# Optimization experiments

Hardware: AMD Instinct MI355X
Metric: run time of the kernel (lower is better)

Reference implementation:

```python
import jax, jax.numpy as jnp
import numpy as np

B, C, H, W = 4, 128, 128, 128
CO = 128           # output channels of deformable conv
KH = KW = 3
K = KH * KW        # 9 kernel taps


def setup_inputs() -> dict:
    key = jax.random.key(0)
    k1, k2, k3, k4 = jax.random.split(key, 4)
    x = jax.random.normal(k1, (B, C, H, W), jnp.float32)
    # conv_offset: Conv2D(3*K channels, 3x3, stride 1, same, bias), channels_first
    offset_w = jax.random.normal(k2, (3 * K, C, KH, KW), jnp.float32) * 0.01
    offset_b = jnp.zeros((3 * K,), jnp.float32)
    # deformable conv weights: [CO, C, KH, KW] + bias
    deform_w = jax.random.normal(k3, (CO, C, KH, KW), jnp.float32) * (1.0 / np.sqrt(C * K))
    deform_b = jax.random.normal(k4, (CO,), jnp.float32) * 0.01
    return {"x": x, "offset_w": offset_w, "offset_b": offset_b,
            "deform_w": deform_w, "deform_b": deform_b}


def _bilinear_gather(x, y, xc):
    """Bilinear sample x [B,C,H,W] at float coords y, xc [B,K,H,W].
    Out-of-bounds samples contribute zero. Returns [B,C,K,H,W]."""
    Bn, Cn, Hn, Wn = x.shape
    y0 = jnp.floor(y)
    x0 = jnp.floor(xc)
    wy = y - y0   # frac weights
    wx = xc - x0
    xf = x.reshape(Bn, Cn, Hn * Wn)

    def corner(yc, xcc, wgt):
        valid = (yc >= 0) & (yc < Hn) & (xcc >= 0) & (xcc < Wn)
        yi = jnp.clip(yc, 0, Hn - 1).astype(jnp.int32)
        xi = jnp.clip(xcc, 0, Wn - 1).astype(jnp.int32)
        idx = (yi * Wn + xi).reshape(Bn, 1, -1)            # [B,1,K*H*W]
        g = jnp.take_along_axis(xf, idx, axis=2)           # [B,C,K*H*W]
        g = g.reshape(Bn, Cn, *yc.shape[1:])               # [B,C,K,H,W]
        return g * (wgt * valid)[:, None]

    return (corner(y0,     x0,     (1 - wy) * (1 - wx))
          + corner(y0,     x0 + 1, (1 - wy) * wx)
          + corner(y0 + 1, x0,     wy * (1 - wx))
          + corner(y0 + 1, x0 + 1, wy * wx))


def reference(x, offset_w, offset_b, deform_w, deform_b):
    # offset/mask predicting conv (stride 1, SAME, channels_first)
    wi = jax.lax.conv_general_dilated(
        x, offset_w, window_strides=(1, 1), padding='SAME',
        dimension_numbers=('NCHW', 'OIHW', 'NCHW')) + offset_b[None, :, None, None]
    o1, o2, m = jnp.split(wi, 3, axis=1)      # each [B,K,H,W]
    dy, dx = o1, o2                            # offset = concat(o1, o2)
    mask = jax.nn.sigmoid(m)

    # kernel tap displacements relative to center (SAME padding, 3x3)
    ky = jnp.repeat(jnp.arange(KH), KW) - (KH // 2)   # [K]
    kx = jnp.tile(jnp.arange(KW), KH) - (KW // 2)     # [K]
    y = dy + jnp.arange(H, dtype=jnp.float32)[None, None, :, None] + ky[None, :, None, None]
    xs = dx + jnp.arange(W, dtype=jnp.float32)[None, None, None, :] + kx[None, :, None, None]

    samp = _bilinear_gather(x, y, xs)          # [B,C,K,H,W]
    # modulated accumulation: sum over ci and kernel taps
    out = jnp.einsum('bckhw,ock->bohw', samp * mask[:, None], deform_w.reshape(CO, C, K))
    return out + deform_b[None, :, None, None]
```

## Files before the change

### kernel.cpp

```cpp
#include <hip/hip_runtime.h>
#include <math.h>

#define Bn 4
#define Cn 128
#define Hn 128
#define Wn 128
#define COn 128
#define HWn (Hn*Wn)
#define NPIX (Bn*HWn)

typedef __attribute__((ext_vector_type(8))) short bf16x8;
typedef __attribute__((ext_vector_type(4))) float f32x4;

__device__ inline short f2bf(float f) {
    union { float f; unsigned u; } cv; cv.f = f;
    unsigned u = cv.u;
    u += 0x7fffu + ((u >> 16) & 1u);
    return (short)(u >> 16);
}
__device__ inline float bflo(unsigned w) {
    union { unsigned u; float f; } cv; cv.u = w << 16; return cv.f;
}
__device__ inline float bfhi(unsigned w) {
    union { unsigned u; float f; } cv; cv.u = w & 0xffff0000u; return cv.f;
}
__device__ inline void async_copy16(const void* g, void* l) {
    __builtin_amdgcn_global_load_lds(
        (const __attribute__((address_space(1))) unsigned int*)g,
        (__attribute__((address_space(3))) unsigned int*)l, 16, 0, 0);
}

__global__ __launch_bounds__(256) void k_transpose(
    const float* __restrict__ x, unsigned short* __restrict__ xt)
{
    __shared__ unsigned short t[Wn][Cn + 2];
    const int tid = threadIdx.x;
    const int bh  = blockIdx.x;
    const int b   = bh >> 7, h = bh & 127;
    const float* xp = x + (((size_t)b*Cn) << 14) + h*Wn;
    for (int i = tid; i < Cn*Wn; i += 256) {
        int c = i >> 7, w = i & 127;
        t[w][c] = (unsigned short)f2bf(xp[(size_t)c*HWn + w]);
    }
    __syncthreads();
    unsigned* xto = (unsigned*)(xt + ((size_t)bh << 7) * Cn);
    for (int j = tid; j < Wn*(Cn/2); j += 256) {
        int w = j >> 6, cp = j & 63;
        xto[(size_t)w*64 + cp] = *(const unsigned*)&t[w][2*cp];
    }
}

__global__ __launch_bounds__(64) void k_pack_w(
    const float* __restrict__ dw, short* __restrict__ pw)
{
    const int blk = blockIdx.x;
    const int ks  = blk >> 3;
    const int ot  = blk & 7;
    const int cchunk = ks / 9;
    const int tap    = ks - cchunk*9;
    const int l   = threadIdx.x;
    const int oc  = ot*16 + (l & 15);
    const int kk0 = (l >> 4)*8;
    bf16x8 fr;
    #pragma unroll
    for (int j = 0; j < 8; ++j) {
        int c = cchunk*32 + kk0 + j;
        fr[j] = f2bf(dw[oc*1152 + c*9 + tap]);
    }
    *(bf16x8*)(pw + ((size_t)blk*64 + l)*8) = fr;
}

__global__ __launch_bounds__(64) void k_pack_ow(
    const float* __restrict__ ow, short* __restrict__ pwo)
{
    const int blk = blockIdx.x;
    const int ks  = blk >> 1;
    const int ot  = blk & 1;
    const int cchunk = ks / 9;
    const int tap    = ks - cchunk*9;
    const int l   = threadIdx.x;
    const int oc  = ot*16 + (l & 15);
    const int kk0 = (l >> 4)*8;
    bf16x8 fr;
    #pragma unroll
    for (int j = 0; j < 8; ++j) {
        int c = cchunk*32 + kk0 + j;
        fr[j] = (oc < 27) ? f2bf(ow[oc*1152 + c*9 + tap]) : (short)0;
    }
    *(bf16x8*)(pwo + ((size_t)blk*64 + l)*8) = fr;
}

__global__ __launch_bounds__(256) void k_offset_mfma(
    const unsigned short* __restrict__ xt, const short* __restrict__ pwo,
    const float* __restrict__ ob, float* __restrict__ offs)
{
    const int tid = threadIdx.x;
    const int wid = tid >> 6;
    const int l   = tid & 63;
    const int lm  = l & 15;
    const int lg  = l >> 4;
    const int bid = blockIdx.x;
    const int wg  = (bid & 7)*128 + (bid >> 3);
    const int p   = wg*64 + wid*16 + lm;
    const int b   = p >> 14;
    const int hw  = p & (HWn - 1);
    const int h   = hw >> 7;
    const int w   = hw & (Wn - 1);

    f32x4 acc[2];
    acc[0] = (f32x4){0.f,0.f,0.f,0.f};
    acc[1] = (f32x4){0.f,0.f,0.f,0.f};
    const int4* apg = (const int4*)pwo;

    #pragma unroll 1
    for (int ks = 0; ks < 36; ++ks) {
        const int cchunk = ks / 9;
        const int tap    = ks - cchunk*9;
        const int y  = h + tap/3 - 1;
        const int xx = w + (tap - (tap/3)*3) - 1;
        const bool ok = (y >= 0) & (y < Hn) & (xx >= 0) & (xx < Wn);
        const int yc  = min(max(y, 0), Hn-1);
        const int xc  = min(max(xx, 0), Wn-1);
        int4 v = *(const int4*)(xt + (((size_t)(b*Hn + yc)*Wn + xc) << 7)
                                   + cchunk*32 + lg*8);
        if (!ok) v = make_int4(0,0,0,0);
        const int4* ap = apg + (size_t)(ks*2)*64 + l;
        acc[0] = __builtin_amdgcn_mfma_f32_16x16x32_bf16(
            __builtin_bit_cast(bf16x8, ap[0]), __builtin_bit_cast(bf16x8, v), acc[0], 0, 0, 0);
        acc[1] = __builtin_amdgcn_mfma_f32_16x16x32_bf16(
            __builtin_bit_cast(bf16x8, ap[64]), __builtin_bit_cast(bf16x8, v), acc[1], 0, 0, 0);
    }

    #pragma unroll
    for (int ot = 0; ot < 2; ++ot)
        #pragma unroll
        for (int r = 0; r < 4; ++r) {
            int oc = ot*16 + lg*4 + r;
            if (oc < 27) offs[(size_t)p*27 + oc] = acc[ot][r] + ob[oc];
        }
}

__global__ __launch_bounds__(256) void k_deform_mfma(
    const unsigned short* __restrict__ xt, const char* __restrict__ pw,
    const float* __restrict__ db, const float* __restrict__ offs,
    float* __restrict__ out)
{
    __shared__ __align__(16) char a_lds[2][8192];
    const int tid = threadIdx.x;
    const int wid = tid >> 6;
    const int l   = tid & 63;
    const int lm  = l & 15;
    const int lg  = l >> 4;
    const int bid = blockIdx.x;
    const int wg  = (bid & 7)*128 + (bid >> 3);
    const int p   = wg*64 + wid*16 + lm;
    const int b   = p >> 14;
    const int hw  = p & (HWn - 1);
    const int h   = hw >> 7;
    const int w   = hw & (Wn - 1);

    f32x4 acc[8];
    #pragma unroll
    for (int ot = 0; ot < 8; ++ot) acc[ot] = (f32x4){0.f,0.f,0.f,0.f};

    const float* op = offs + (size_t)p * 27;
    const int rowbase = b*Hn;

    #define STAGE(ks_, buf_) {                                                  \
        const char* g0 = pw + (size_t)(ks_)*8192 + wid*1024 + l*16;             \
        async_copy16(g0,        (void*)&a_lds[buf_][wid*1024]);                 \
        async_copy16(g0 + 4096, (void*)&a_lds[buf_][4096 + wid*1024]);          \
    }

    STAGE(0, 0);
    int cur = 0;

    #pragma unroll 1
    for (int ks = 0; ks < 36; ++ks) {
        const int cchunk = ks / 9;
        const int tap    = ks - cchunk*9;
        __syncthreads();
        if (ks + 1 < 36) STAGE(ks + 1, cur ^ 1);

        float dy = op[tap], dx = op[9 + tap], mr = op[18 + tap];
        float m  = 1.0f / (1.0f + __expf(-mr));
        float yf = (float)(h + tap/3 - 1) + dy;
        float xf = (float)(w + (tap - (tap/3)*3) - 1) + dx;
        float y0f = floorf(yf), x0f = floorf(xf);
        int   y0  = (int)y0f,  x0  = (int)x0f;
        float wy = yf - y0f, wx = xf - x0f;
        int yi0 = min(max(y0,     0), Hn-1), yi1 = min(max(y0 + 1, 0), Hn-1);
        int xi0 = min(max(x0,     0), Wn-1), xi1 = min(max(x0 + 1, 0), Wn-1);
        float vy0 = ((y0 >= 0)     & (y0 < Hn))     ? 1.0f : 0.0f;
        float vy1 = ((y0 + 1 >= 0) & (y0 + 1 < Hn)) ? 1.0f : 0.0f;
        float vx0 = ((x0 >= 0)     & (x0 < Wn))     ? 1.0f : 0.0f;
        float vx1 = ((x0 + 1 >= 0) & (x0 + 1 < Wn)) ? 1.0f : 0.0f;
        const float w0_ = m * (1.0f-wy) * (1.0f-wx) * vy0 * vx0;
        const float w1_ = m * (1.0f-wy) * wx        * vy0 * vx1;
        const float w2_ = m * wy        * (1.0f-wx) * vy1 * vx0;
        const float w3_ = m * wy        * wx        * vy1 * vx1;

        const int cb = cchunk*32 + lg*8;
        const uint4 q0 = *(const uint4*)(xt + (((size_t)((rowbase + yi0)*Wn + xi0)) << 7) + cb);
        const uint4 q1 = *(const uint4*)(xt + (((size_t)((rowbase + yi0)*Wn + xi1)) << 7) + cb);
        const uint4 q2 = *(const uint4*)(xt + (((size_t)((rowbase + yi1)*Wn + xi0)) << 7) + cb);
        const uint4 q3 = *(const uint4*)(xt + (((size_t)((rowbase + yi1)*Wn + xi1)) << 7) + cb);

        unsigned bw[4];
        const unsigned* u0 = (const unsigned*)&q0;
        const unsigned* u1 = (const unsigned*)&q1;
        const unsigned* u2 = (const unsigned*)&q2;
        const unsigned* u3 = (const unsigned*)&q3;
        #pragma unroll
        for (int q = 0; q < 4; ++q) {
            float lo = w0_*bflo(u0[q]) + w1_*bflo(u1[q]) + w2_*bflo(u2[q]) + w3_*bflo(u3[q]);
            float hi = w0_*bfhi(u0[q]) + w1_*bfhi(u1[q]) + w2_*bfhi(u2[q]) + w3_*bfhi(u3[q]);
            bw[q] = ((unsigned)(unsigned short)f2bf(hi) << 16) | (unsigned short)f2bf(lo);
        }
        int4 bi = make_int4(bw[0], bw[1], bw[2], bw[3]);
        bf16x8 bfrag = __builtin_bit_cast(bf16x8, bi);

        #pragma unroll
        for (int ot = 0; ot < 8; ++ot) {
            int4 av = *(const int4*)&a_lds[cur][(ot*64 + l)*16];
            acc[ot] = __builtin_amdgcn_mfma_f32_16x16x32_bf16(
                __builtin_bit_cast(bf16x8, av), bfrag, acc[ot], 0, 0, 0);
        }
        cur ^= 1;
    }

    #pragma unroll
    for (int ot = 0; ot < 8; ++ot) {
        #pragma unroll
        for (int r = 0; r < 4; ++r) {
            int oc = ot*16 + lg*4 + r;
            out[((size_t)(b*COn + oc) << 14) + hw] = acc[ot][r] + db[oc];
        }
    }
    #undef STAGE
}

extern "C" void kernel_launch(void* const* d_in, const int* in_sizes, int n_in,
                              void* d_out, int out_size, void* d_ws, size_t ws_size,
                              hipStream_t stream) {
    const float* x  = (const float*)d_in[0];
    const float* ow = (const float*)d_in[1];
    const float* ob = (const float*)d_in[2];
    const float* dw = (const float*)d_in[3];
    const float* db = (const float*)d_in[4];
    float* out  = (float*)d_out;

    float*          offs = (float*)d_ws;
    short*          pw   = (short*)((char*)d_ws + 7077888);
    short*          pwo  = (short*)((char*)d_ws + 7372800);
    unsigned short* xtp  = (unsigned short*)((char*)d_ws + 7446528);

    hipLaunchKernelGGL(k_transpose,   dim3(Bn*Hn),    dim3(256), 0, stream, x, xtp);
    hipLaunchKernelGGL(k_pack_w,      dim3(288),      dim3(64),  0, stream, dw, pw);
    hipLaunchKernelGGL(k_pack_ow,     dim3(72),       dim3(64),  0, stream, ow, pwo);
    hipLaunchKernelGGL(k_offset_mfma, dim3(NPIX/64),  dim3(256), 0, stream, xtp, pwo, ob, offs);
    hipLaunchKernelGGL(k_deform_mfma, dim3(NPIX/64),  dim3(256), 0, stream,
                       xtp, (const char*)pw, db, offs, out);
}
```

Measured before the change: 137.4 us.

## Reorder K loop tap-major so bilinear coords are computed once per tap

The reduction loop now runs over taps outermost with the four 32-channel chunks innermost. Packed weights are reordered to match the new tap-major index. Offset, mask and bilinear weights are computed once per tap instead of once per chunk, and the four corner gathers for one pixel hit consecutive channel chunks, which should improve locality. The software bf16 conversion is also replaced with the HIP intrinsic, which may lower to a hardware convert; rounding should stay round-to-nearest-even.

```diff
diff --git a/kernel.cpp b/kernel.cpp
--- a/kernel.cpp
+++ b/kernel.cpp
@@ -1,4 +1,5 @@
 #include <hip/hip_runtime.h>
+#include <hip/hip_bf16.h>
 #include <math.h>
 
 #define Bn 4
@@ -12,11 +13,15 @@
 typedef __attribute__((ext_vector_type(8))) short bf16x8;
 typedef __attribute__((ext_vector_type(4))) float f32x4;
 
-__device__ inline short f2bf(float f) {
-    union { float f; unsigned u; } cv; cv.f = f;
-    unsigned u = cv.u;
-    u += 0x7fffu + ((u >> 16) & 1u);
-    return (short)(u >> 16);
+__device__ inline unsigned short f2bf_hw(float f) {
+    __hip_bfloat16 h = __float2bfloat16(f);
+    return *reinterpret_cast<unsigned short*>(&h);
+}
+__device__ inline unsigned pack_bf2(float lo, float hi) {
+    __hip_bfloat162 h2;
+    h2.x = __float2bfloat16(lo);
+    h2.y = __float2bfloat16(hi);
+    return *reinterpret_cast<unsigned*>(&h2);
 }
 __device__ inline float bflo(unsigned w) {
     union { unsigned u; float f; } cv; cv.u = w << 16; return cv.f;
@@ -40,7 +45,7 @@
     const float* xp = x + (((size_t)b*Cn) << 14) + h*Wn;
     for (int i = tid; i < Cn*Wn; i += 256) {
         int c = i >> 7, w = i & 127;
-        t[w][c] = (unsigned short)f2bf(xp[(size_t)c*HWn + w]);
+        t[w][c] = f2bf_hw(xp[(size_t)c*HWn + w]);
     }
     __syncthreads();
     unsigned* xto = (unsigned*)(xt + ((size_t)bh << 7) * Cn);
@@ -56,16 +61,16 @@
     const int blk = blockIdx.x;
     const int ks  = blk >> 3;
     const int ot  = blk & 7;
-    const int cchunk = ks / 9;
-    const int tap    = ks - cchunk*9;
+    const int tap = ks >> 2;
+    const int cq  = ks & 3;
     const int l   = threadIdx.x;
     const int oc  = ot*16 + (l & 15);
     const int kk0 = (l >> 4)*8;
     bf16x8 fr;
     #pragma unroll
     for (int j = 0; j < 8; ++j) {
-        int c = cchunk*32 + kk0 + j;
-        fr[j] = f2bf(dw[oc*1152 + c*9 + tap]);
+        int c = cq*32 + kk0 + j;
+        fr[j] = (short)f2bf_hw(dw[oc*1152 + c*9 + tap]);
     }
     *(bf16x8*)(pw + ((size_t)blk*64 + l)*8) = fr;
 }
@@ -76,16 +81,16 @@
     const int blk = blockIdx.x;
     const int ks  = blk >> 1;
     const int ot  = blk & 1;
-    const int cchunk = ks / 9;
-    const int tap    = ks - cchunk*9;
+    const int tap = ks >> 2;
+    const int cq  = ks & 3;
     const int l   = threadIdx.x;
     const int oc  = ot*16 + (l & 15);
     const int kk0 = (l >> 4)*8;
     bf16x8 fr;
     #pragma unroll
     for (int j = 0; j < 8; ++j) {
-        int c = cchunk*32 + kk0 + j;
-        fr[j] = (oc < 27) ? f2bf(ow[oc*1152 + c*9 + tap]) : (short)0;
+        int c = cq*32 + kk0 + j;
+        fr[j] = (oc < 27) ? (short)f2bf_hw(ow[oc*1152 + c*9 + tap]) : (short)0;
     }
     *(bf16x8*)(pwo + ((size_t)blk*64 + l)*8) = fr;
 }
@@ -113,22 +118,25 @@
     const int4* apg = (const int4*)pwo;
 
     #pragma unroll 1
-    for (int ks = 0; ks < 36; ++ks) {
-        const int cchunk = ks / 9;
-        const int tap    = ks - cchunk*9;
+    for (int tap = 0; tap < 9; ++tap) {
         const int y  = h + tap/3 - 1;
         const int xx = w + (tap - (tap/3)*3) - 1;
         const bool ok = (y >= 0) & (y < Hn) & (xx >= 0) & (xx < Wn);
         const int yc  = min(max(y, 0), Hn-1);
         const int xc  = min(max(xx, 0), Wn-1);
-        int4 v = *(const int4*)(xt + (((size_t)(b*Hn + yc)*Wn + xc) << 7)
-                                   + cchunk*32 + lg*8);
-        if (!ok) v = make_int4(0,0,0,0);
-        const int4* ap = apg + (size_t)(ks*2)*64 + l;
-        acc[0] = __builtin_amdgcn_mfma_f32_16x16x32_bf16(
-            __builtin_bit_cast(bf16x8, ap[0]), __builtin_bit_cast(bf16x8, v), acc[0], 0, 0, 0);
-        acc[1] = __builtin_amdgcn_mfma_f32_16x16x32_bf16(
-            __builtin_bit_cast(bf16x8, ap[64]), __builtin_bit_cast(bf16x8, v), acc[1], 0, 0, 0);
+        const unsigned short* bp =
+            xt + (((size_t)((b*Hn + yc)*Wn + xc)) << 7) + lg*8;
+        #pragma unroll
+        for (int cq = 0; cq < 4; ++cq) {
+            int4 v = *(const int4*)(bp + cq*32);
+            if (!ok) v = make_int4(0,0,0,0);
+            const int ks = tap*4 + cq;
+            const int4* ap = apg + (size_t)(ks*2)*64 + l;
+            acc[0] = __builtin_amdgcn_mfma_f32_16x16x32_bf16(
+                __builtin_bit_cast(bf16x8, ap[0]),  __builtin_bit_cast(bf16x8, v), acc[0], 0, 0, 0);
+            acc[1] = __builtin_amdgcn_mfma_f32_16x16x32_bf16(
+                __builtin_bit_cast(bf16x8, ap[64]), __builtin_bit_cast(bf16x8, v), acc[1], 0, 0, 0);
+        }
     }
 
     #pragma unroll
@@ -176,12 +184,7 @@
     int cur = 0;
 
     #pragma unroll 1
-    for (int ks = 0; ks < 36; ++ks) {
-        const int cchunk = ks / 9;
-        const int tap    = ks - cchunk*9;
-        __syncthreads();
-        if (ks + 1 < 36) STAGE(ks + 1, cur ^ 1);
-
+    for (int tap = 0; tap < 9; ++tap) {
         float dy = op[tap], dx = op[9 + tap], mr = op[18 + tap];
         float m  = 1.0f / (1.0f + __expf(-mr));
         float yf = (float)(h + tap/3 - 1) + dy;
@@ -200,33 +203,44 @@
         const float w2_ = m * wy        * (1.0f-wx) * vy1 * vx0;
         const float w3_ = m * wy        * wx        * vy1 * vx1;
 
-        const int cb = cchunk*32 + lg*8;
-        const uint4 q0 = *(const uint4*)(xt + (((size_t)((rowbase + yi0)*Wn + xi0)) << 7) + cb);
-        const uint4 q1 = *(const uint4*)(xt + (((size_t)((rowbase + yi0)*Wn + xi1)) << 7) + cb);
-        const uint4 q2 = *(const uint4*)(xt + (((size_t)((rowbase + yi1)*Wn + xi0)) << 7) + cb);
-        const uint4 q3 = *(const uint4*)(xt + (((size_t)((rowbase + yi1)*Wn + xi1)) << 7) + cb);
-
-        unsigned bw[4];
-        const unsigned* u0 = (const unsigned*)&q0;
-        const unsigned* u1 = (const unsigned*)&q1;
-        const unsigned* u2 = (const unsigned*)&q2;
-        const unsigned* u3 = (const unsigned*)&q3;
-        #pragma unroll
-        for (int q = 0; q < 4; ++q) {
-            float lo = w0_*bflo(u0[q]) + w1_*bflo(u1[q]) + w2_*bflo(u2[q]) + w3_*bflo(u3[q]);
-            float hi = w0_*bfhi(u0[q]) + w1_*bfhi(u1[q]) + w2_*bfhi(u2[q]) + w3_*bfhi(u3[q]);
-            bw[q] = ((unsigned)(unsigned short)f2bf(hi) << 16) | (unsigned short)f2bf(lo);
-        }
-        int4 bi = make_int4(bw[0], bw[1], bw[2], bw[3]);
-        bf16x8 bfrag = __builtin_bit_cast(bf16x8, bi);
-
-        #pragma unroll
-        for (int ot = 0; ot < 8; ++ot) {
-            int4 av = *(const int4*)&a_lds[cur][(ot*64 + l)*16];
-            acc[ot] = __builtin_amdgcn_mfma_f32_16x16x32_bf16(
-                __builtin_bit_cast(bf16x8, av), bfrag, acc[ot], 0, 0, 0);
-        }
-        cur ^= 1;
+        const unsigned short* c00 = xt + (((size_t)((rowbase + yi0)*Wn + xi0)) << 7) + lg*8;
+        const unsigned short* c01 = xt + (((size_t)((rowbase + yi0)*Wn + xi1)) << 7) + lg*8;
+        const unsigned short* c10 = xt + (((size_t)((rowbase + yi1)*Wn + xi0)) << 7) + lg*8;
+        const unsigned short* c11 = xt + (((size_t)((rowbase + yi1)*Wn + xi1)) << 7) + lg*8;
+
+        #pragma unroll
+        for (int cq = 0; cq < 4; ++cq) {
+            const int ks = tap*4 + cq;
+            __syncthreads();
+            if (ks + 1 < 36) STAGE(ks + 1, cur ^ 1);
+
+            const uint4 q0 = *(const uint4*)(c00 + cq*32);
+            const uint4 q1 = *(const uint4*)(c01 + cq*32);
+            const uint4 q2 = *(const uint4*)(c10 + cq*32);
+            const uint4 q3 = *(const uint4*)(c11 + cq*32);
+
+            unsigned bw[4];
+            const unsigned* u0 = (const unsigned*)&q0;
+            const unsigned* u1 = (const unsigned*)&q1;
+            const unsigned* u2 = (const unsigned*)&q2;
+            const unsigned* u3 = (const unsigned*)&q3;
+            #pragma unroll
+            for (int q = 0; q < 4; ++q) {
+                float lo = w0_*bflo(u0[q]) + w1_*bflo(u1[q]) + w2_*bflo(u2[q]) + w3_*bflo(u3[q]);
+                float hi = w0_*bfhi(u0[q]) + w1_*bfhi(u1[q]) + w2_*bfhi(u2[q]) + w3_*bfhi(u3[q]);
+                bw[q] = pack_bf2(lo, hi);
+            }
+            int4 bi = make_int4(bw[0], bw[1], bw[2], bw[3]);
+            bf16x8 bfrag = __builtin_bit_cast(bf16x8, bi);
+
+            #pragma unroll
+            for (int ot = 0; ot < 8; ++ot) {
+                int4 av = *(const int4*)&a_lds[cur][(ot*64 + l)*16];
+                acc[ot] = __builtin_amdgcn_mfma_f32_16x16x32_bf16(
+                    __builtin_bit_cast(bf16x8, av), bfrag, acc[ot], 0, 0, 0);
+            }
+            cur ^= 1;
+        }
     }
 
     #pragma unroll
```

After: 151.1 us. 10.0% more time.

## Split deform conv K-loop across two wave groups with LDS reduction

Applied to the files above, without the earlier changes.

The deformable conv kernel now runs 512 threads per block. Two groups of four waves each handle half of the 36 k-steps, each with its own double-buffered weight staging in LDS, and the partial accumulators are summed through LDS before the output store. This doubles the waves working on each 64-pixel tile, shortening the serial gather-plus-MFMA chain per wave and adding latency hiding, at the cost of double the LDS, a reduction step, and idle waves during the store. The manual float-to-bf16 rounding is also replaced with the HIP intrinsic conversion, which may lower to hardware pack instructions.

```diff
diff --git a/kernel.cpp b/kernel.cpp
--- a/kernel.cpp
+++ b/kernel.cpp
@@ -1,4 +1,5 @@
 #include <hip/hip_runtime.h>
+#include <hip/hip_bf16.h>
 #include <math.h>
 
 #define Bn 4
@@ -12,11 +13,15 @@
 typedef __attribute__((ext_vector_type(8))) short bf16x8;
 typedef __attribute__((ext_vector_type(4))) float f32x4;
 
-__device__ inline short f2bf(float f) {
-    union { float f; unsigned u; } cv; cv.f = f;
-    unsigned u = cv.u;
-    u += 0x7fffu + ((u >> 16) & 1u);
-    return (short)(u >> 16);
+__device__ inline unsigned short f2bf_hw(float f) {
+    __hip_bfloat16 h = __float2bfloat16(f);
+    return *reinterpret_cast<unsigned short*>(&h);
+}
+__device__ inline unsigned pack_bf2(float lo, float hi) {
+    __hip_bfloat162 h2;
+    h2.x = __float2bfloat16(lo);
+    h2.y = __float2bfloat16(hi);
+    return *reinterpret_cast<unsigned*>(&h2);
 }
 __device__ inline float bflo(unsigned w) {
     union { unsigned u; float f; } cv; cv.u = w << 16; return cv.f;
@@ -40,7 +45,7 @@
     const float* xp = x + (((size_t)b*Cn) << 14) + h*Wn;
     for (int i = tid; i < Cn*Wn; i += 256) {
         int c = i >> 7, w = i & 127;
-        t[w][c] = (unsigned short)f2bf(xp[(size_t)c*HWn + w]);
+        t[w][c] = f2bf_hw(xp[(size_t)c*HWn + w]);
     }
     __syncthreads();
     unsigned* xto = (unsigned*)(xt + ((size_t)bh << 7) * Cn);
@@ -65,7 +70,7 @@
     #pragma unroll
     for (int j = 0; j < 8; ++j) {
         int c = cchunk*32 + kk0 + j;
-        fr[j] = f2bf(dw[oc*1152 + c*9 + tap]);
+        fr[j] = (short)f2bf_hw(dw[oc*1152 + c*9 + tap]);
     }
     *(bf16x8*)(pw + ((size_t)blk*64 + l)*8) = fr;
 }
@@ -85,7 +90,7 @@
     #pragma unroll
     for (int j = 0; j < 8; ++j) {
         int c = cchunk*32 + kk0 + j;
-        fr[j] = (oc < 27) ? f2bf(ow[oc*1152 + c*9 + tap]) : (short)0;
+        fr[j] = (oc < 27) ? (short)f2bf_hw(ow[oc*1152 + c*9 + tap]) : (short)0;
     }
     *(bf16x8*)(pwo + ((size_t)blk*64 + l)*8) = fr;
 }
@@ -126,7 +131,7 @@
         if (!ok) v = make_int4(0,0,0,0);
         const int4* ap = apg + (size_t)(ks*2)*64 + l;
         acc[0] = __builtin_amdgcn_mfma_f32_16x16x32_bf16(
-            __builtin_bit_cast(bf16x8, ap[0]), __builtin_bit_cast(bf16x8, v), acc[0], 0, 0, 0);
+            __builtin_bit_cast(bf16x8, ap[0]),  __builtin_bit_cast(bf16x8, v), acc[0], 0, 0, 0);
         acc[1] = __builtin_amdgcn_mfma_f32_16x16x32_bf16(
             __builtin_bit_cast(bf16x8, ap[64]), __builtin_bit_cast(bf16x8, v), acc[1], 0, 0, 0);
     }
@@ -140,24 +145,26 @@
         }
 }
 
-__global__ __launch_bounds__(256) void k_deform_mfma(
+__global__ __launch_bounds__(512, 8) void k_deform_mfma(
     const unsigned short* __restrict__ xt, const char* __restrict__ pw,
     const float* __restrict__ db, const float* __restrict__ offs,
     float* __restrict__ out)
 {
-    __shared__ __align__(16) char a_lds[2][8192];
-    const int tid = threadIdx.x;
-    const int wid = tid >> 6;
-    const int l   = tid & 63;
-    const int lm  = l & 15;
-    const int lg  = l >> 4;
-    const int bid = blockIdx.x;
-    const int wg  = (bid & 7)*128 + (bid >> 3);
-    const int p   = wg*64 + wid*16 + lm;
-    const int b   = p >> 14;
-    const int hw  = p & (HWn - 1);
-    const int h   = hw >> 7;
-    const int w   = hw & (Wn - 1);
+    __shared__ __align__(16) char a_lds[2][2][8192];
+    const int tid  = threadIdx.x;
+    const int wid  = tid >> 6;
+    const int gid  = wid >> 2;
+    const int wsub = wid & 3;
+    const int l    = tid & 63;
+    const int lm   = l & 15;
+    const int lg   = l >> 4;
+    const int bid  = blockIdx.x;
+    const int wg   = (bid & 7)*128 + (bid >> 3);
+    const int p    = wg*64 + wsub*16 + lm;
+    const int b    = p >> 14;
+    const int hw   = p & (HWn - 1);
+    const int h    = hw >> 7;
+    const int w    = hw & (Wn - 1);
 
     f32x4 acc[8];
     #pragma unroll
@@ -165,22 +172,24 @@
 
     const float* op = offs + (size_t)p * 27;
     const int rowbase = b*Hn;
+    const int ks0 = gid*18;
 
     #define STAGE(ks_, buf_) {                                                  \
-        const char* g0 = pw + (size_t)(ks_)*8192 + wid*1024 + l*16;             \
-        async_copy16(g0,        (void*)&a_lds[buf_][wid*1024]);                 \
-        async_copy16(g0 + 4096, (void*)&a_lds[buf_][4096 + wid*1024]);          \
-    }
-
-    STAGE(0, 0);
+        const char* g0 = pw + (size_t)(ks_)*8192 + wsub*1024 + l*16;            \
+        async_copy16(g0,        (void*)&a_lds[gid][buf_][wsub*1024]);           \
+        async_copy16(g0 + 4096, (void*)&a_lds[gid][buf_][4096 + wsub*1024]);    \
+    }
+
+    STAGE(ks0, 0);
     int cur = 0;
 
     #pragma unroll 1
-    for (int ks = 0; ks < 36; ++ks) {
+    for (int s = 0; s < 18; ++s) {
+        const int ks     = ks0 + s;
         const int cchunk = ks / 9;
         const int tap    = ks - cchunk*9;
         __syncthreads();
-        if (ks + 1 < 36) STAGE(ks + 1, cur ^ 1);
+        if (s + 1 < 18) STAGE(ks + 1, cur ^ 1);
 
         float dy = op[tap], dx = op[9 + tap], mr = op[18 + tap];
         float m  = 1.0f / (1.0f + __expf(-mr));
@@ -215,29 +224,40 @@
         for (int q = 0; q < 4; ++q) {
             float lo = w0_*bflo(u0[q]) + w1_*bflo(u1[q]) + w2_*bflo(u2[q]) + w3_*bflo(u3[q]);
             float hi = w0_*bfhi(u0[q]) + w1_*bfhi(u1[q]) + w2_*bfhi(u2[q]) + w3_*bfhi(u3[q]);
-            bw[q] = ((unsigned)(unsigned short)f2bf(hi) << 16) | (unsigned short)f2bf(lo);
+            bw[q] = pack_bf2(lo, hi);
         }
         int4 bi = make_int4(bw[0], bw[1], bw[2], bw[3]);
         bf16x8 bfrag = __builtin_bit_cast(bf16x8, bi);
 
         #pragma unroll
         for (int ot = 0; ot < 8; ++ot) {
-            int4 av = *(const int4*)&a_lds[cur][(ot*64 + l)*16];
+            int4 av = *(const int4*)&a_lds[gid][cur][(ot*64 + l)*16];
             acc[ot] = __builtin_amdgcn_mfma_f32_16x16x32_bf16(
                 __builtin_bit_cast(bf16x8, av), bfrag, acc[ot], 0, 0, 0);
         }
         cur ^= 1;
     }
-
-    #pragma unroll
-    for (int ot = 0; ot < 8; ++ot) {
-        #pragma unroll
-        for (int r = 0; r < 4; ++r) {
-            int oc = ot*16 + lg*4 + r;
-            out[((size_t)(b*COn + oc) << 14) + hw] = acc[ot][r] + db[oc];
-        }
-    }
     #undef STAGE
+
+    __syncthreads();
+    float4* red = (float4*)a_lds;
+    if (gid == 1) {
+        #pragma unroll
+        for (int ot = 0; ot < 8; ++ot)
+            red[(wsub*8 + ot)*64 + l] = (float4){acc[ot][0], acc[ot][1], acc[ot][2], acc[ot][3]};
+    }
+    __syncthreads();
+    if (gid == 0) {
+        #pragma unroll
+        for (int ot = 0; ot < 8; ++ot) {
+            float4 o2 = red[(wsub*8 + ot)*64 + l];
+            #pragma unroll
+            for (int r = 0; r < 4; ++r) {
+                int oc = ot*16 + lg*4 + r;
+                out[((size_t)(b*COn + oc) << 14) + hw] = acc[ot][r] + (&o2.x)[r] + db[oc];
+            }
+        }
+    }
 }
 
 extern "C" void kernel_launch(void* const* d_in, const int* in_sizes, int n_in,
@@ -259,6 +279,6 @@
     hipLaunchKernelGGL(k_pack_w,      dim3(288),      dim3(64),  0, stream, dw, pw);
     hipLaunchKernelGGL(k_pack_ow,     dim3(72),       dim3(64),  0, stream, ow, pwo);
     hipLaunchKernelGGL(k_offset_mfma, dim3(NPIX/64),  dim3(256), 0, stream, xtp, pwo, ob, offs);
-    hipLaunchKernelGGL(k_deform_mfma, dim3(NPIX/64),  dim3(256), 0, stream,
+    hipLaunchKernelGGL(k_deform_mfma, dim3(NPIX/64),  dim3(512), 0, stream,
                        xtp, (const char*)pw, db, offs, out);
 }
```

Result: slower. 184.6 us (+34.3%).

## Precompute bilinear sampling metadata in offset kernel, use hardware bf16 conversion

Applied to the files above, without the earlier changes.

The offset conv kernel now stages its outputs in LDS and computes per-pixel, per-tap sampling metadata: a base byte offset, neighbour step flags, and four bf16-packed bilinear weights with the mask folded in. This replaces the float offset buffer. The deform kernel previously redid this sigmoid, floor and clamp work for each of the 4 channel chunks; it now loads one 16-byte record per tap instead. Float-to-bf16 conversion also switches to the HIP intrinsic, which may map to a packed hardware convert. The cost is that bilinear weights are quantized to bf16, a small precision change, and the metadata buffer is larger than the old offsets buffer.

```diff
diff --git a/kernel.cpp b/kernel.cpp
--- a/kernel.cpp
+++ b/kernel.cpp
@@ -1,4 +1,5 @@
 #include <hip/hip_runtime.h>
+#include <hip/hip_bf16.h>
 #include <math.h>
 
 #define Bn 4
@@ -12,11 +13,15 @@
 typedef __attribute__((ext_vector_type(8))) short bf16x8;
 typedef __attribute__((ext_vector_type(4))) float f32x4;
 
-__device__ inline short f2bf(float f) {
-    union { float f; unsigned u; } cv; cv.f = f;
-    unsigned u = cv.u;
-    u += 0x7fffu + ((u >> 16) & 1u);
-    return (short)(u >> 16);
+__device__ inline unsigned short f2bf_hw(float f) {
+    __hip_bfloat16 h = __float2bfloat16(f);
+    return *reinterpret_cast<unsigned short*>(&h);
+}
+__device__ inline unsigned pack_bf2(float lo, float hi) {
+    __hip_bfloat162 h2;
+    h2.x = __float2bfloat16(lo);
+    h2.y = __float2bfloat16(hi);
+    return *reinterpret_cast<unsigned*>(&h2);
 }
 __device__ inline float bflo(unsigned w) {
     union { unsigned u; float f; } cv; cv.u = w << 16; return cv.f;
@@ -40,7 +45,7 @@
     const float* xp = x + (((size_t)b*Cn) << 14) + h*Wn;
     for (int i = tid; i < Cn*Wn; i += 256) {
         int c = i >> 7, w = i & 127;
-        t[w][c] = (unsigned short)f2bf(xp[(size_t)c*HWn + w]);
+        t[w][c] = f2bf_hw(xp[(size_t)c*HWn + w]);
     }
     __syncthreads();
     unsigned* xto = (unsigned*)(xt + ((size_t)bh << 7) * Cn);
@@ -65,7 +70,7 @@
     #pragma unroll
     for (int j = 0; j < 8; ++j) {
         int c = cchunk*32 + kk0 + j;
-        fr[j] = f2bf(dw[oc*1152 + c*9 + tap]);
+        fr[j] = (short)f2bf_hw(dw[oc*1152 + c*9 + tap]);
     }
     *(bf16x8*)(pw + ((size_t)blk*64 + l)*8) = fr;
 }
@@ -85,15 +90,16 @@
     #pragma unroll
     for (int j = 0; j < 8; ++j) {
         int c = cchunk*32 + kk0 + j;
-        fr[j] = (oc < 27) ? f2bf(ow[oc*1152 + c*9 + tap]) : (short)0;
+        fr[j] = (oc < 27) ? (short)f2bf_hw(ow[oc*1152 + c*9 + tap]) : (short)0;
     }
     *(bf16x8*)(pwo + ((size_t)blk*64 + l)*8) = fr;
 }
 
 __global__ __launch_bounds__(256) void k_offset_mfma(
     const unsigned short* __restrict__ xt, const short* __restrict__ pwo,
-    const float* __restrict__ ob, float* __restrict__ offs)
-{
+    const float* __restrict__ ob, uint4* __restrict__ meta)
+{
+    __shared__ float ol[4][16][33];
     const int tid = threadIdx.x;
     const int wid = tid >> 6;
     const int l   = tid & 63;
@@ -126,7 +132,7 @@
         if (!ok) v = make_int4(0,0,0,0);
         const int4* ap = apg + (size_t)(ks*2)*64 + l;
         acc[0] = __builtin_amdgcn_mfma_f32_16x16x32_bf16(
-            __builtin_bit_cast(bf16x8, ap[0]), __builtin_bit_cast(bf16x8, v), acc[0], 0, 0, 0);
+            __builtin_bit_cast(bf16x8, ap[0]),  __builtin_bit_cast(bf16x8, v), acc[0], 0, 0, 0);
         acc[1] = __builtin_amdgcn_mfma_f32_16x16x32_bf16(
             __builtin_bit_cast(bf16x8, ap[64]), __builtin_bit_cast(bf16x8, v), acc[1], 0, 0, 0);
     }
@@ -136,13 +142,48 @@
         #pragma unroll
         for (int r = 0; r < 4; ++r) {
             int oc = ot*16 + lg*4 + r;
-            if (oc < 27) offs[(size_t)p*27 + oc] = acc[ot][r] + ob[oc];
-        }
+            ol[wid][lm][oc] = acc[ot][r] + ((oc < 27) ? ob[oc] : 0.0f);
+        }
+
+    const int pbase = wg*64 + wid*16;
+    for (int i = l; i < 144; i += 64) {
+        const int tap = i >> 4;
+        const int px  = i & 15;
+        const int pp  = pbase + px;
+        const int bb  = pp >> 14;
+        const int hh  = (pp & (HWn-1)) >> 7;
+        const int ww  = pp & 127;
+        float dy = ol[wid][px][tap];
+        float dx = ol[wid][px][9 + tap];
+        float mr = ol[wid][px][18 + tap];
+        float m  = 1.0f / (1.0f + __expf(-mr));
+        float yf = (float)(hh + tap/3 - 1) + dy;
+        float xf = (float)(ww + (tap - (tap/3)*3) - 1) + dx;
+        float y0f = floorf(yf), x0f = floorf(xf);
+        int   y0  = (int)y0f,  x0  = (int)x0f;
+        float wy = yf - y0f, wx = xf - x0f;
+        int yi0 = min(max(y0,     0), Hn-1), yi1 = min(max(y0 + 1, 0), Hn-1);
+        int xi0 = min(max(x0,     0), Wn-1), xi1 = min(max(x0 + 1, 0), Wn-1);
+        float vy0 = ((y0 >= 0)     & (y0 < Hn))     ? 1.0f : 0.0f;
+        float vy1 = ((y0 + 1 >= 0) & (y0 + 1 < Hn)) ? 1.0f : 0.0f;
+        float vx0 = ((x0 >= 0)     & (x0 < Wn))     ? 1.0f : 0.0f;
+        float vx1 = ((x0 + 1 >= 0) & (x0 + 1 < Wn)) ? 1.0f : 0.0f;
+        float w0_ = m * (1.0f-wy) * (1.0f-wx) * vy0 * vx0;
+        float w1_ = m * (1.0f-wy) * wx        * vy0 * vx1;
+        float w2_ = m * wy        * (1.0f-wx) * vy1 * vx0;
+        float w3_ = m * wy        * wx        * vy1 * vx1;
+        uint4 mq;
+        mq.x = (unsigned)(((bb << 14) + yi0*Wn + xi0) << 8);
+        mq.y = (unsigned)((xi1 - xi0)*256) | (unsigned)((yi1 - yi0)*32768);
+        mq.z = pack_bf2(w0_, w1_);
+        mq.w = pack_bf2(w2_, w3_);
+        meta[(size_t)tap*NPIX + pp] = mq;
+    }
 }
 
 __global__ __launch_bounds__(256) void k_deform_mfma(
     const unsigned short* __restrict__ xt, const char* __restrict__ pw,
-    const float* __restrict__ db, const float* __restrict__ offs,
+    const float* __restrict__ db, const uint4* __restrict__ meta,
     float* __restrict__ out)
 {
     __shared__ __align__(16) char a_lds[2][8192];
@@ -156,15 +197,13 @@
     const int p   = wg*64 + wid*16 + lm;
     const int b   = p >> 14;
     const int hw  = p & (HWn - 1);
-    const int h   = hw >> 7;
-    const int w   = hw & (Wn - 1);
 
     f32x4 acc[8];
     #pragma unroll
     for (int ot = 0; ot < 8; ++ot) acc[ot] = (f32x4){0.f,0.f,0.f,0.f};
 
-    const float* op = offs + (size_t)p * 27;
-    const int rowbase = b*Hn;
+    const uint4* mbase = meta + p;
+    const char*  xb    = (const char*)xt;
 
     #define STAGE(ks_, buf_) {                                                  \
         const char* g0 = pw + (size_t)(ks_)*8192 + wid*1024 + l*16;             \
@@ -182,29 +221,18 @@
         __syncthreads();
         if (ks + 1 < 36) STAGE(ks + 1, cur ^ 1);
 
-        float dy = op[tap], dx = op[9 + tap], mr = op[18 + tap];
-        float m  = 1.0f / (1.0f + __expf(-mr));
-        float yf = (float)(h + tap/3 - 1) + dy;
-        float xf = (float)(w + (tap - (tap/3)*3) - 1) + dx;
-        float y0f = floorf(yf), x0f = floorf(xf);
-        int   y0  = (int)y0f,  x0  = (int)x0f;
-        float wy = yf - y0f, wx = xf - x0f;
-        int yi0 = min(max(y0,     0), Hn-1), yi1 = min(max(y0 + 1, 0), Hn-1);
-        int xi0 = min(max(x0,     0), Wn-1), xi1 = min(max(x0 + 1, 0), Wn-1);
-        float vy0 = ((y0 >= 0)     & (y0 < Hn))     ? 1.0f : 0.0f;
-        float vy1 = ((y0 + 1 >= 0) & (y0 + 1 < Hn)) ? 1.0f : 0.0f;
-        float vx0 = ((x0 >= 0)     & (x0 < Wn))     ? 1.0f : 0.0f;
-        float vx1 = ((x0 + 1 >= 0) & (x0 + 1 < Wn)) ? 1.0f : 0.0f;
-        const float w0_ = m * (1.0f-wy) * (1.0f-wx) * vy0 * vx0;
-        const float w1_ = m * (1.0f-wy) * wx        * vy0 * vx1;
-        const float w2_ = m * wy        * (1.0f-wx) * vy1 * vx0;
-        const float w3_ = m * wy        * wx        * vy1 * vx1;
-
-        const int cb = cchunk*32 + lg*8;
-        const uint4 q0 = *(const uint4*)(xt + (((size_t)((rowbase + yi0)*Wn + xi0)) << 7) + cb);
-        const uint4 q1 = *(const uint4*)(xt + (((size_t)((rowbase + yi0)*Wn + xi1)) << 7) + cb);
-        const uint4 q2 = *(const uint4*)(xt + (((size_t)((rowbase + yi1)*Wn + xi0)) << 7) + cb);
-        const uint4 q3 = *(const uint4*)(xt + (((size_t)((rowbase + yi1)*Wn + xi1)) << 7) + cb);
+        const uint4 mq = mbase[(size_t)tap*NPIX];
+        const unsigned offc = mq.x + (unsigned)(cchunk*64 + lg*16);
+        const unsigned dxb  = mq.y & 256u;
+        const unsigned dyb  = mq.y & 32768u;
+
+        const uint4 q0 = *(const uint4*)(xb + offc);
+        const uint4 q1 = *(const uint4*)(xb + (offc + dxb));
+        const uint4 q2 = *(const uint4*)(xb + (offc + dyb));
+        const uint4 q3 = *(const uint4*)(xb + (offc + dyb + dxb));
+
+        const float w0_ = bflo(mq.z), w1_ = bfhi(mq.z);
+        const float w2_ = bflo(mq.w), w3_ = bfhi(mq.w);
 
         unsigned bw[4];
         const unsigned* u0 = (const unsigned*)&q0;
@@ -215,7 +243,7 @@
         for (int q = 0; q < 4; ++q) {
             float lo = w0_*bflo(u0[q]) + w1_*bflo(u1[q]) + w2_*bflo(u2[q]) + w3_*bflo(u3[q]);
             float hi = w0_*bfhi(u0[q]) + w1_*bfhi(u1[q]) + w2_*bfhi(u2[q]) + w3_*bfhi(u3[q]);
-            bw[q] = ((unsigned)(unsigned short)f2bf(hi) << 16) | (unsigned short)f2bf(lo);
+            bw[q] = pack_bf2(lo, hi);
         }
         int4 bi = make_int4(bw[0], bw[1], bw[2], bw[3]);
         bf16x8 bfrag = __builtin_bit_cast(bf16x8, bi);
@@ -228,6 +256,7 @@
         }
         cur ^= 1;
     }
+    #undef STAGE
 
     #pragma unroll
     for (int ot = 0; ot < 8; ++ot) {
@@ -237,7 +266,6 @@
             out[((size_t)(b*COn + oc) << 14) + hw] = acc[ot][r] + db[oc];
         }
     }
-    #undef STAGE
 }
 
 extern "C" void kernel_launch(void* const* d_in, const int* in_sizes, int n_in,
@@ -250,15 +278,15 @@
     const float* db = (const float*)d_in[4];
     float* out  = (float*)d_out;
 
-    float*          offs = (float*)d_ws;
-    short*          pw   = (short*)((char*)d_ws + 7077888);
-    short*          pwo  = (short*)((char*)d_ws + 7372800);
-    unsigned short* xtp  = (unsigned short*)((char*)d_ws + 7446528);
+    uint4*          meta = (uint4*)d_ws;
+    short*          pw   = (short*)((char*)d_ws + 9437184);
+    short*          pwo  = (short*)((char*)d_ws + 9732096);
+    unsigned short* xtp  = (unsigned short*)((char*)d_ws + 9805824);
 
     hipLaunchKernelGGL(k_transpose,   dim3(Bn*Hn),    dim3(256), 0, stream, x, xtp);
     hipLaunchKernelGGL(k_pack_w,      dim3(288),      dim3(64),  0, stream, dw, pw);
     hipLaunchKernelGGL(k_pack_ow,     dim3(72),       dim3(64),  0, stream, ow, pwo);
-    hipLaunchKernelGGL(k_offset_mfma, dim3(NPIX/64),  dim3(256), 0, stream, xtp, pwo, ob, offs);
+    hipLaunchKernelGGL(k_offset_mfma, dim3(NPIX/64),  dim3(256), 0, stream, xtp, pwo, ob, meta);
     hipLaunchKernelGGL(k_deform_mfma, dim3(NPIX/64),  dim3(256), 0, stream,
-                       xtp, (const char*)pw, db, offs, out);
-}
+                       xtp, (const char*)pw, db, meta, out);
+}
```

Result: faster. 124.4 us (-9.5%).
